# Kernel optimization log

Hardware: AMD Instinct MI355X
Metric: run time of the kernel (lower is better)

Reference implementation:

```python
import jax, jax.numpy as jnp
import numpy as np

B, H, W = 32, 512, 512
LAM = 1.0


def _pdist(x):
    # x: (n, d) -> (n, n) euclidean distance matrix (torch.cdist equivalent)
    sq = jnp.sum(x * x, axis=-1)
    d2 = sq[:, None] + sq[None, :] - 2.0 * (x @ x.T)
    return jnp.sqrt(jnp.maximum(d2, 0.0))


def _mst_edges(D):
    # 0-dim Vietoris-Rips persistence pairing == edges of the minimum spanning
    # tree of the distance matrix. Prim's algorithm, n-1 sequential steps.
    n = D.shape[0]
    big = jnp.asarray(jnp.finfo(D.dtype).max, D.dtype)
    in_tree = jnp.zeros(n, dtype=bool).at[0].set(True)
    min_dist = D[0].at[0].set(big)          # best distance from tree to each node
    min_from = jnp.zeros(n, dtype=jnp.int32)  # tree endpoint achieving min_dist

    def step(carry, _):
        in_tree, md, mf = carry
        j = jnp.argmin(jnp.where(in_tree, big, md)).astype(jnp.int32)
        i = mf[j]
        in_tree = in_tree.at[j].set(True)
        better = (D[j] < md) & (~in_tree)
        md = jnp.where(better, D[j], md)
        mf = jnp.where(better, j, mf)
        return (in_tree, md, mf), (i, j)

    _, (us, vs) = jax.lax.scan(step, (in_tree, min_dist, min_from), None, length=n - 1)
    return us, vs  # each (n-1,) int32


def _topo_loss_single(x, z):
    # x, z: (n, d) point clouds (prediction / mask rows as points)
    Dx = _pdist(x)
    Dz = _pdist(z)
    # SignatureLoss normalisation: divide distance matrices by their max
    Dx = Dx / jnp.maximum(Dx.max(), 1e-12)
    Dz = Dz / jnp.maximum(Dz.max(), 1e-12)
    # persistence pairings (dim 0) of each space
    ux, vx = _mst_edges(jax.lax.stop_gradient(Dx))
    uz, vz = _mst_edges(jax.lax.stop_gradient(Dz))
    # signature loss (Topological Autoencoders, p=2):
    # ||D_X[pi_X] - D_Z[pi_X]||_2^2 + ||D_X[pi_Z] - D_Z[pi_Z]||_2^2
    t1 = jnp.sum((Dx[ux, vx] - Dz[ux, vx]) ** 2)
    t2 = jnp.sum((Dx[uz, vz] - Dz[uz, vz]) ** 2)
    return t1 + t2


def setup_inputs() -> dict:
    key = jax.random.key(0)
    k1, k2 = jax.random.split(key)
    model_output = jax.random.normal(k1, (B, 1, H, W), dtype=jnp.float32)
    labels = jax.random.uniform(k2, (B, 1, H, W), dtype=jnp.float32)
    return {"model_output": model_output, "labels": labels}


def reference(model_output, labels):
    preds = jax.nn.sigmoid(jnp.squeeze(model_output, axis=1))  # (B, H, W)
    masks = jnp.squeeze(labels, axis=1)                        # (B, H, W)
    losses = jax.vmap(_topo_loss_single)(preds, masks)         # (B,)
    return LAM * jnp.sum(losses) / preds.shape[0]
```

## Files before the change

kernel.cpp:

```cpp
#include <hip/hip_runtime.h>
#include <math.h>

#define NN 512
#define NN2 (NN*NN)
#define NB 32
#define NM 64

typedef __attribute__((ext_vector_type(8))) short short8v;
typedef __attribute__((ext_vector_type(4))) float f32x4;

typedef const unsigned int __attribute__((address_space(1)))* gas_ptr;
typedef unsigned int __attribute__((address_space(3)))* las_ptr;

__device__ __forceinline__ float sigm(float x) { return 1.0f / (1.0f + expf(-x)); }

__device__ __forceinline__ unsigned short f2bf(float x) {
  unsigned u = __float_as_uint(x);
  return (unsigned short)((u + 0x7fffu + ((u >> 16) & 1u)) >> 16);
}
__device__ __forceinline__ float bf2f(unsigned short h) {
  return __uint_as_float(((unsigned)h) << 16);
}
__device__ __forceinline__ unsigned long long u64min(unsigned long long a,
                                                     unsigned long long b) {
  return (b < a) ? b : a;
}
__device__ __forceinline__ void amin64(unsigned long long* p, unsigned long long v) {
  unsigned long long old = *p;
  while (v < old) {
    unsigned long long assumed = old;
    old = atomicCAS(p, assumed, v);
    if (old == assumed) break;
  }
}
template <int CTRL>
__device__ __forceinline__ unsigned long long dpp_min_u64(unsigned long long x) {
  int xlo = (int)(unsigned)x, xhi = (int)(unsigned)(x >> 32);
  int ylo = __builtin_amdgcn_update_dpp(xlo, xlo, CTRL, 0xf, 0xf, false);
  int yhi = __builtin_amdgcn_update_dpp(xhi, xhi, CTRL, 0xf, 0xf, false);
  unsigned long long y = ((unsigned long long)(unsigned)yhi << 32) | (unsigned)ylo;
  return (y < x) ? y : x;
}
__device__ __forceinline__ unsigned long long wave_min_u64(unsigned long long k) {
  k = dpp_min_u64<0x111>(k); k = dpp_min_u64<0x112>(k);
  k = dpp_min_u64<0x114>(k); k = dpp_min_u64<0x118>(k);
  k = dpp_min_u64<0x142>(k); k = dpp_min_u64<0x143>(k);
  return k;
}
__device__ __forceinline__ unsigned long long grp16_min_u64(unsigned long long k) {
  k = dpp_min_u64<0x111>(k); k = dpp_min_u64<0x112>(k);
  k = dpp_min_u64<0x114>(k); k = dpp_min_u64<0x118>(k);
  return k;
}

__global__ __launch_bounds__(256) void split_kernel(const float* __restrict__ model,
                                                    const float* __restrict__ labels,
                                                    unsigned short* __restrict__ Hi,
                                                    unsigned short* __restrict__ Lo,
                                                    float* __restrict__ sq, int m0) {
  int b = blockIdx.x;
  int mL = b >> 8;
  int m = m0 + mL;
  int tid = threadIdx.x;
  size_t off = (size_t)(b & 255) * 1024 + tid * 4;
  const float* src = ((m & 1) ? labels + (size_t)(m >> 1) * NN2
                              : model + (size_t)(m >> 1) * NN2) + off;
  float4 v = *(const float4*)src;
  if (!(m & 1)) { v.x = sigm(v.x); v.y = sigm(v.y); v.z = sigm(v.z); v.w = sigm(v.w); }
  ushort4 h, l;
  h.x = f2bf(v.x); l.x = f2bf(v.x - bf2f(h.x));
  h.y = f2bf(v.y); l.y = f2bf(v.y - bf2f(h.y));
  h.z = f2bf(v.z); l.z = f2bf(v.z - bf2f(h.z));
  h.w = f2bf(v.w); l.w = f2bf(v.w - bf2f(h.w));
  *(ushort4*)(Hi + (size_t)mL * NN2 + off) = h;
  *(ushort4*)(Lo + (size_t)mL * NN2 + off) = l;
  float s = v.x * v.x + v.y * v.y + v.z * v.z + v.w * v.w;
  #pragma unroll
  for (int o = 32; o > 0; o >>= 1) s += __shfl_down(s, o);
  __shared__ float red[4];
  if ((tid & 63) == 0) red[tid >> 6] = s;
  __syncthreads();
  if (tid == 0) {
    int row0 = (b & 255) * 2;
    sq[(size_t)m * NN + row0]     = red[0] + red[1];
    sq[(size_t)m * NN + row0 + 1] = red[2] + red[3];
  }
}

__global__ __launch_bounds__(256, 3) void gemm_dist(const unsigned short* __restrict__ Hi,
                                                    const unsigned short* __restrict__ Lo,
                                                    const float* __restrict__ sq,
                                                    unsigned short* __restrict__ Dreg,
                                                    unsigned* __restrict__ maxBits,
                                                    unsigned long long* __restrict__ best1,
                                                    int m0, int nm) {
  __shared__ unsigned short P[4][4096];
  int id = blockIdx.x;
  int p, mL;
  if ((nm & 7) == 0) {
    int x = id & 7, t = id >> 3;
    p = t % 10;
    mL = x + 8 * (t / 10);
  } else {
    p = id % 10;
    mL = id / 10;
  }
  int by = (p >= 4) + (p >= 7) + (p >= 9);
  int bx = p - ((by * (7 - by)) >> 1);
  bool diag = (by == bx);
  int m = m0 + mL;
  const unsigned short* Hm = Hi + (size_t)mL * NN2;
  const unsigned short* Lm = Lo + (size_t)mL * NN2;

  int tid = threadIdx.x;
  int wid = tid >> 6, lane = tid & 63;
  int wy = wid >> 1, wx = wid & 1;
  int lr = lane & 15, lk = lane >> 4;

  const unsigned short* wsrcM = (wid & 1) ? Lm : Hm;
  int wrow0 = (wid < 2) ? by * 128 : bx * 128;
  bool stage = (!diag) || (wid < 2);
  int srow = lane >> 2;
  int schunk = (lane & 3) ^ ((lane >> 3) & 3);
  const unsigned short* gsrc = wsrcM + (size_t)(wrow0 + srow) * NN + schunk * 8;
  unsigned short* ldst = &P[wid & 3][0];

  f32x4 acc[4][4];
  #pragma unroll
  for (int i = 0; i < 4; ++i)
    #pragma unroll
    for (int j = 0; j < 4; ++j) acc[i][j] = (f32x4){0.f, 0.f, 0.f, 0.f};

  const unsigned short* bAh = &P[0][0];
  const unsigned short* bAl = &P[1][0];
  const unsigned short* bBh = diag ? &P[0][0] : &P[2][0];
  const unsigned short* bBl = diag ? &P[1][0] : &P[3][0];
  int sw = (lr >> 1) & 3;
  int rao = (wy * 64 + lr) * 32 + (lk ^ sw) * 8;
  int rbo = (wx * 64 + lr) * 32 + (lk ^ sw) * 8;

  for (int s = 0; s < 16; ++s) {
    int k0 = s * 32;
    if (stage) {
      #pragma unroll
      for (int i = 0; i < 8; ++i)
        __builtin_amdgcn_global_load_lds(
            (gas_ptr)(const void*)(gsrc + k0 + (size_t)i * 16 * NN),
            (las_ptr)(void*)(ldst + i * 512), 16, 0, 0);
    }
    __syncthreads();

    short8v fa[4], fb[4], fb2[4];
    #pragma unroll
    for (int i = 0; i < 4; ++i) {
      fa[i] = *(const short8v*)(bAh + rao + i * 512);
      fb[i] = *(const short8v*)(bBh + rbo + i * 512);
    }
    #pragma unroll
    for (int mi = 0; mi < 4; ++mi)
      #pragma unroll
      for (int ni = 0; ni < 4; ++ni)
        acc[mi][ni] = __builtin_amdgcn_mfma_f32_16x16x32_bf16(fa[mi], fb[ni], acc[mi][ni], 0, 0, 0);
    #pragma unroll
    for (int i = 0; i < 4; ++i)
      fb2[i] = *(const short8v*)(bBl + rbo + i * 512);
    #pragma unroll
    for (int mi = 0; mi < 4; ++mi)
      #pragma unroll
      for (int ni = 0; ni < 4; ++ni)
        acc[mi][ni] = __builtin_amdgcn_mfma_f32_16x16x32_bf16(fa[mi], fb2[ni], acc[mi][ni], 0, 0, 0);
    #pragma unroll
    for (int i = 0; i < 4; ++i)
      fa[i] = *(const short8v*)(bAl + rao + i * 512);
    #pragma unroll
    for (int mi = 0; mi < 4; ++mi)
      #pragma unroll
      for (int ni = 0; ni < 4; ++ni)
        acc[mi][ni] = __builtin_amdgcn_mfma_f32_16x16x32_bf16(fa[mi], fb[ni], acc[mi][ni], 0, 0, 0);
    __syncthreads();
  }

  const float* sqm = sq + (size_t)m * NN;
  unsigned short* Dm = Dreg + (size_t)mL * NN2;
  int gr0 = by * 128 + wy * 64;
  int gc0 = bx * 128 + wx * 64;
  unsigned hmax = 0;
  unsigned long long* b1 = best1 + (size_t)m * NN;
  unsigned long long ck[4];
  #pragma unroll
  for (int i = 0; i < 4; ++i) ck[i] = ~0ull;
  unsigned short us[4][4][4];

  #pragma unroll
  for (int mi = 0; mi < 4; ++mi) {
    int rb = gr0 + mi * 16 + lk * 4;
    float sqi0 = sqm[rb + 0], sqi1 = sqm[rb + 1], sqi2 = sqm[rb + 2], sqi3 = sqm[rb + 3];
    unsigned long long rk[4];
    #pragma unroll
    for (int j = 0; j < 4; ++j) rk[j] = ~0ull;
    #pragma unroll
    for (int ni = 0; ni < 4; ++ni) {
      int col = gc0 + ni * 16 + lr;
      float sqj = sqm[col];
      f32x4 a = acc[mi][ni];
      unsigned short h0 = f2bf(sqrtf(fmaxf(sqi0 + sqj - 2.f * a[0], 0.f)));
      unsigned short h1 = f2bf(sqrtf(fmaxf(sqi1 + sqj - 2.f * a[1], 0.f)));
      unsigned short h2 = f2bf(sqrtf(fmaxf(sqi2 + sqj - 2.f * a[2], 0.f)));
      unsigned short h3 = f2bf(sqrtf(fmaxf(sqi3 + sqj - 2.f * a[3], 0.f)));
      us[mi][ni][0] = h0; us[mi][ni][1] = h1;
      us[mi][ni][2] = h2; us[mi][ni][3] = h3;
      unsigned hm01 = (h0 > h1) ? h0 : h1;
      unsigned hm23 = (h2 > h3) ? h2 : h3;
      unsigned hm = (hm01 > hm23) ? hm01 : hm23;
      hmax = (hm > hmax) ? hm : hmax;
      unsigned short hh[4] = {h0, h1, h2, h3};
      #pragma unroll
      for (int rg = 0; rg < 4; ++rg) {
        int row = rb + rg;
        if (!diag || col != row) {
          unsigned lo = (row < col) ? (unsigned)(row * NN + col)
                                    : (unsigned)(col * NN + row);
          unsigned long long key = ((unsigned long long)hh[rg] << 48) | lo;
          rk[rg] = u64min(rk[rg], key);
          ck[ni] = u64min(ck[ni], key);
        }
      }
    }
    #pragma unroll
    for (int rg = 0; rg < 4; ++rg) {
      unsigned long long k = grp16_min_u64(rk[rg]);
      if (lr == 15) atomicMin(&b1[rb + rg], k);
    }
  }
  if (!diag) {
    #pragma unroll
    for (int ni = 0; ni < 4; ++ni) {
      unsigned long long k = ck[ni];
      k = u64min(k, __shfl_xor(k, 16));
      k = u64min(k, __shfl_xor(k, 32));
      if (lk == 0) atomicMin(&b1[gc0 + ni * 16 + lr], k);
    }
  }

  __syncthreads();
  unsigned short* W = &P[0][0] + wid * 1216;
  int rlo = lane >> 4, cq = lane & 15;
  #pragma unroll
  for (int mi = 0; mi < 4; ++mi) {
    #pragma unroll
    for (int ni = 0; ni < 4; ++ni)
      #pragma unroll
      for (int j = 0; j < 4; ++j)
        W[(lk * 4 + j) * 76 + ni * 16 + lr] = us[mi][ni][j];
    #pragma unroll
    for (int g = 0; g < 4; ++g) {
      int r16 = g * 4 + rlo;
      ushort4 t = *(const ushort4*)&W[r16 * 76 + cq * 4];
      *(ushort4*)(Dm + (size_t)(gr0 + mi * 16 + r16) * NN + gc0 + cq * 4) = t;
    }
  }
  if (!diag) {
    #pragma unroll
    for (int ni = 0; ni < 4; ++ni) {
      #pragma unroll
      for (int mi = 0; mi < 4; ++mi)
        *(ushort4*)&W[lr * 76 + mi * 16 + lk * 4] =
            make_ushort4(us[mi][ni][0], us[mi][ni][1], us[mi][ni][2], us[mi][ni][3]);
      #pragma unroll
      for (int g = 0; g < 4; ++g) {
        int r16 = g * 4 + rlo;
        ushort4 t = *(const ushort4*)&W[r16 * 76 + cq * 4];
        *(ushort4*)(Dm + (size_t)(gc0 + ni * 16 + r16) * NN + gr0 + cq * 4) = t;
      }
    }
  }

  #pragma unroll
  for (int off = 32; off > 0; off >>= 1) {
    unsigned o = (unsigned)__shfl_down((int)hmax, off);
    hmax = (o > hmax) ? o : hmax;
  }
  if (lane == 0) atomicMax(&maxBits[m], hmax << 16);
}

__global__ __launch_bounds__(512) void scan2_kernel(const unsigned short* __restrict__ Dreg,
                                                    const unsigned long long* __restrict__ best1,
                                                    int* __restrict__ compG,
                                                    unsigned long long* __restrict__ best2,
                                                    unsigned long long* __restrict__ DcG,
                                                    int2* __restrict__ eo_all,
                                                    int* __restrict__ ecntG, int m0) {
  int sblk = blockIdx.x, mL = blockIdx.y, m = m0 + mL;
  const unsigned short* D = Dreg + (size_t)mL * NN2;
  __shared__ int compP[NN + 64];
  __shared__ int hook[NN], parent[NN];
  __shared__ int ecnt;
  int tid = threadIdx.x;
  int wave = tid >> 6, lane = tid & 63;
  int c0 = lane * 8;

  unsigned long long* dginit = DcG + (size_t)mL * 16384 + sblk * 2048;
  #pragma unroll
  for (int i = 0; i < 4; ++i) dginit[tid + i * 512] = ~0ull;

  if (tid == 0) ecnt = 0;
  unsigned long long b = best1[(size_t)m * NN + tid];
  int h;
  if (b != ~0ull) {
    int idx = (int)(unsigned)b & 0x3ffff;
    int er = idx >> 9, ec = idx & 511;
    h = (er == tid) ? ec : er;
  } else h = tid;
  hook[tid] = h;
  __syncthreads();
  bool active = (b != ~0ull);
  int p = h;
  bool mutual = active && (hook[p] == tid);
  parent[tid] = (!active) ? tid : ((mutual && tid < p) ? tid : p);
  if (sblk == 0 && active && (!mutual || tid > p)) {
    int idx = (int)(unsigned)b & 0x3ffff;
    int e = atomicAdd(&ecnt, 1);
    eo_all[(size_t)m * (NN - 1) + e] = make_int2(idx >> 9, idx & 511);
  }
  __syncthreads();
  int c = tid, pp = parent[c];
  while (pp != c) { c = pp; pp = parent[c]; }
  compP[tid + (tid >> 3)] = c;
  if (sblk == 0) {
    compG[(size_t)m * NN + tid] = c;
    if (tid == 0) ecntG[m] = ecnt;
  }
  __syncthreads();

  unsigned long long* b2 = best2 + (size_t)m * NN;
  #pragma unroll
  for (int rr = 0; rr < 8; ++rr) {
    int r = sblk * 64 + wave * 8 + rr;
    int cr = compP[r + (r >> 3)];
    uint4 dv = *(const uint4*)(D + (size_t)r * NN + c0);
    int4 cc0 = *(const int4*)(compP + c0 + (c0 >> 3));
    int4 cc1 = *(const int4*)(compP + c0 + 4 + (c0 >> 3));
    unsigned hh[8] = {dv.x & 0xffffu, dv.x >> 16, dv.y & 0xffffu, dv.y >> 16,
                      dv.z & 0xffffu, dv.z >> 16, dv.w & 0xffffu, dv.w >> 16};
    int cv[8] = {cc0.x, cc0.y, cc0.z, cc0.w, cc1.x, cc1.y, cc1.z, cc1.w};
    unsigned long long k = ~0ull;
    #pragma unroll
    for (int e = 0; e < 8; ++e) {
      if (cv[e] != cr) {
        int col = c0 + e;
        int lo = (r < col) ? r * NN + col : col * NN + r;
        unsigned long long key = ((unsigned long long)hh[e] << 48) | (unsigned)lo;
        k = u64min(k, key);
      }
    }
    k = wave_min_u64(k);
    if (lane == 63 && k != ~0ull) atomicMin(&b2[cr], k);
  }
}

__global__ __launch_bounds__(512) void hook2_kernel(const unsigned long long* __restrict__ best2,
                                                    const int* __restrict__ compG,
                                                    int* __restrict__ comp2g,
                                                    int2* __restrict__ eo_all,
                                                    int* __restrict__ ecntG,
                                                    int* __restrict__ cntG, int m0) {
  int mL = blockIdx.x, m = m0 + mL;
  const unsigned long long* b2 = best2 + (size_t)m * NN;
  int2* eo = eo_all + (size_t)m * (NN - 1);
  __shared__ int comp[NN], hook[NN], parent[NN], dmap[NN];
  __shared__ int ecnt, ccnt;
  int tid = threadIdx.x;
  if (tid == 0) { ecnt = ecntG[m]; ccnt = 0; }
  comp[tid] = compG[(size_t)m * NN + tid];
  __syncthreads();
  unsigned long long b = b2[tid];
  int h;
  if (b != ~0ull) {
    int idx = (int)(unsigned)b & 0x3ffff;
    int er = idx >> 9, ec = idx & 511;
    int c1 = comp[er], c2 = comp[ec];
    h = (c1 == tid) ? c2 : c1;
  } else h = tid;
  hook[tid] = h;
  __syncthreads();
  bool active = (b != ~0ull);
  int p = h;
  bool mutual = active && (hook[p] == tid);
  parent[tid] = (!active) ? tid : ((mutual && tid < p) ? tid : p);
  if (active && (!mutual || tid > p)) {
    int idx = (int)(unsigned)b & 0x3ffff;
    int e = atomicAdd(&ecnt, 1);
    eo[e] = make_int2(idx >> 9, idx & 511);
  }
  __syncthreads();
  int c = comp[tid], pp = parent[c];
  while (pp != c) { c = pp; pp = parent[c]; }
  __syncthreads();
  comp[tid] = c;
  __syncthreads();
  if (comp[tid] == tid) dmap[tid] = atomicAdd(&ccnt, 1);
  __syncthreads();
  comp2g[(size_t)m * NN + tid] = dmap[comp[tid]];
  if (tid == 0) { ecntG[m] = ecnt; cntG[m] = ccnt; }
}

__global__ __launch_bounds__(512) void contract_kernel(const unsigned short* __restrict__ Dreg,
                                                       const int* __restrict__ comp2g,
                                                       unsigned long long* __restrict__ DcG,
                                                       int m0) {
  int q = blockIdx.x, mL = blockIdx.y, m = m0 + mL;
  const unsigned short* D = Dreg + (size_t)mL * NN2;
  __shared__ unsigned long long Dc[128 * 128];
  __shared__ int c2P[NN + 64];
  int tid = threadIdx.x;
  int wave = tid >> 6, lane = tid & 63;
  int c0 = lane * 8;
  if (tid < NN) c2P[tid + (tid >> 3)] = comp2g[(size_t)m * NN + tid];
  for (int i = tid; i < 16384; i += 512) Dc[i] = ~0ull;
  __syncthreads();
  #pragma unroll
  for (int rr = 0; rr < 16; ++rr) {
    int r = q * 128 + wave * 16 + rr;
    int di = c2P[r + (r >> 3)];
    uint4 dv = *(const uint4*)(D + (size_t)r * NN + c0);
    int4 cc0 = *(const int4*)(c2P + c0 + (c0 >> 3));
    int4 cc1 = *(const int4*)(c2P + c0 + 4 + (c0 >> 3));
    unsigned hh[8] = {dv.x & 0xffffu, dv.x >> 16, dv.y & 0xffffu, dv.y >> 16,
                      dv.z & 0xffffu, dv.z >> 16, dv.w & 0xffffu, dv.w >> 16};
    int cv[8] = {cc0.x, cc0.y, cc0.z, cc0.w, cc1.x, cc1.y, cc1.z, cc1.w};
    #pragma unroll
    for (int e = 0; e < 8; ++e) {
      if (cv[e] != di) {
        int col = c0 + e;
        int lo = (r < col) ? r * NN + col : col * NN + r;
        unsigned long long key = ((unsigned long long)hh[e] << 48) | (unsigned)lo;
        amin64(&Dc[di * 128 + cv[e]], key);
      }
    }
  }
  __syncthreads();
  unsigned long long* dg = DcG + (size_t)mL * 16384;
  for (int i = tid; i < 16384; i += 512) {
    unsigned long long v = Dc[i];
    if (v != ~0ull) atomicMin(&dg[i], v);
  }
}

__global__ __launch_bounds__(1024) void finish_kernel(const unsigned short* __restrict__ Dreg,
                                                      const unsigned long long* __restrict__ DcG,
                                                      const int* __restrict__ comp2g,
                                                      const int* __restrict__ cntG,
                                                      int2* __restrict__ eo_all,
                                                      int* __restrict__ ecntG,
                                                      const unsigned* __restrict__ maxBits,
                                                      float* __restrict__ out, int m0) {
  int mL = blockIdx.x, m = m0 + mL;
  __shared__ unsigned long long Dc[16384];
  __shared__ int c2n[NN];
  __shared__ unsigned long long best[128];
  __shared__ int comp2[128], hook128[128], parent128[128];
  __shared__ float fred[16];
  __shared__ int ecnt;
  int tid = threadIdx.x;
  int wave = tid >> 6, lane = tid & 63;
  const unsigned long long* dg = DcG + (size_t)mL * 16384;
  for (int i = tid; i < 16384; i += 1024) Dc[i] = dg[i];
  if (tid < NN) c2n[tid] = comp2g[(size_t)m * NN + tid];
  if (tid < 128) comp2[tid] = tid;
  if (tid == 0) ecnt = ecntG[m];
  __syncthreads();
  int C = cntG[m];
  int2* eo = eo_all + (size_t)m * (NN - 1);

  for (int ph = 0; ph < 7; ++ph) {
    if (ecnt >= NN - 1) break;
    if (tid < 128) best[tid] = ~0ull;
    __syncthreads();
    for (int i = tid; i < C * 128; i += 1024) {
      unsigned long long key = Dc[i];
      if (key == ~0ull) continue;
      int a = i >> 7, bb = i & 127;
      int ca = comp2[a], cb = comp2[bb];
      if (ca != cb) amin64(&best[ca], key);
    }
    __syncthreads();
    if (tid < C) {
      unsigned long long b = best[tid];
      int h;
      if (b != ~0ull) {
        int pid = (int)(unsigned)b & 0x3ffff;
        int er = pid >> 9, ec = pid & 511;
        int c1 = comp2[c2n[er]], c2v = comp2[c2n[ec]];
        h = (c1 == tid) ? c2v : c1;
      } else h = tid;
      hook128[tid] = h;
    }
    __syncthreads();
    if (tid < C) {
      unsigned long long b = best[tid];
      bool active = (b != ~0ull);
      int p = hook128[tid];
      bool mutual = active && (hook128[p] == tid);
      parent128[tid] = (!active) ? tid : ((mutual && tid < p) ? tid : p);
      if (active && (!mutual || tid > p)) {
        int pid = (int)(unsigned)b & 0x3ffff;
        int e = atomicAdd(&ecnt, 1);
        eo[e] = make_int2(pid >> 9, pid & 511);
      }
    }
    __syncthreads();
    if (tid < C) {
      int c = comp2[tid], pp = parent128[c];
      while (pp != c) { c = pp; pp = parent128[c]; }
      comp2[tid] = c;
    }
    __syncthreads();
  }
  __syncthreads();

  int b = m >> 1;
  float mxX = fmaxf(__uint_as_float(maxBits[2 * b]), 1e-12f);
  float mxZ = fmaxf(__uint_as_float(maxBits[2 * b + 1]), 1e-12f);
  float rX = 1.0f / mxX, rZ = 1.0f / mxZ;
  const unsigned short* Dx = Dreg + (size_t)(mL & ~1) * NN2;
  const unsigned short* Dz = Dx + NN2;
  float acc = 0.f;
  if (tid < NN - 1) {
    int2 e = eo[tid];
    size_t off = (size_t)e.x * NN + e.y;
    float d = bf2f(Dx[off]) * rX - bf2f(Dz[off]) * rZ;
    acc = d * d;
  }
  #pragma unroll
  for (int o = 32; o > 0; o >>= 1) acc += __shfl_down(acc, o);
  if (lane == 0) fred[wave] = acc;
  __syncthreads();
  if (tid == 0) {
    float t = 0.f;
    #pragma unroll
    for (int i = 0; i < 16; ++i) t += fred[i];
    atomicAdd(out, t * (1.0f / NB));
  }
}

extern "C" void kernel_launch(void* const* d_in, const int* in_sizes, int n_in,
                              void* d_out, int out_size, void* d_ws, size_t ws_size,
                              hipStream_t stream) {
  const float* model = (const float*)d_in[0];
  const float* labels = (const float*)d_in[1];
  float* out = (float*)d_out;
  char* ws = (char*)d_ws;

  float*              sq      = (float*)(ws);
  unsigned*           maxBits = (unsigned*)(ws + 131072);
  int2*               eo      = (int2*)(ws + 132096);
  unsigned long long* best1   = (unsigned long long*)(ws + 393728);
  unsigned long long* best2   = (unsigned long long*)(ws + 655872);
  int*                compG   = (int*)(ws + 918016);
  int*                comp2g  = (int*)(ws + 1049088);
  int*                ecntG   = (int*)(ws + 1180160);
  int*                cntG    = (int*)(ws + 1180416);
  size_t base = 1181696;

  size_t perBatch = 2ull * (NN2 * 2 + 2ull * NN2 * 2 + 16384 * 8);
  size_t dcap = (ws_size > base) ? (ws_size - base) : 0;
  int cb = (int)(dcap / perBatch);
  if (cb > NB) cb = NB;
  if (cb < 1) cb = 1;
  int nmc = 2 * cb;

  unsigned short* Dreg = (unsigned short*)(ws + base);
  unsigned short* Hi = Dreg + (size_t)nmc * NN2;
  unsigned short* Lo = Hi + (size_t)nmc * NN2;
  unsigned long long* DcG = (unsigned long long*)(Lo + (size_t)nmc * NN2);

  hipMemsetAsync(d_out, 0, sizeof(float), stream);
  hipMemsetAsync(maxBits, 0, 64 * sizeof(unsigned), stream);

  for (int b0 = 0; b0 < NB; b0 += cb) {
    int nb = (NB - b0 < cb) ? (NB - b0) : cb;
    int nm = 2 * nb, m0 = 2 * b0;
    hipMemsetAsync(best1 + (size_t)m0 * NN, 0xFF, (size_t)nm * NN * 16, stream);
    split_kernel<<<nm * 256, 256, 0, stream>>>(model, labels, Hi, Lo, sq, m0);
    gemm_dist<<<10 * nm, 256, 0, stream>>>(Hi, Lo, sq, Dreg, maxBits, best1, m0, nm);
    scan2_kernel<<<dim3(8, nm), 512, 0, stream>>>(Dreg, best1, compG, best2, DcG,
                                                  eo, ecntG, m0);
    hook2_kernel<<<nm, 512, 0, stream>>>(best2, compG, comp2g, eo, ecntG, cntG, m0);
    contract_kernel<<<dim3(4, nm), 512, 0, stream>>>(Dreg, comp2g, DcG, m0);
    finish_kernel<<<nm, 1024, 0, stream>>>(Dreg, DcG, comp2g, cntG, eo, ecntG,
                                           maxBits, out, m0);
  }
}
```

Baseline: 140.3 us.

## Fuse hook2 into contract and finish kernels, fold best-buffer reset into split

```diff
diff --git a/kernel.cpp b/kernel.cpp
--- a/kernel.cpp
+++ b/kernel.cpp
@@ -57,7 +57,10 @@
                                                     const float* __restrict__ labels,
                                                     unsigned short* __restrict__ Hi,
                                                     unsigned short* __restrict__ Lo,
-                                                    float* __restrict__ sq, int m0) {
+                                                    float* __restrict__ sq,
+                                                    unsigned long long* __restrict__ best1,
+                                                    unsigned long long* __restrict__ best2,
+                                                    int m0) {
   int b = blockIdx.x;
   int mL = b >> 8;
   int m = m0 + mL;
@@ -74,6 +77,13 @@
   h.w = f2bf(v.w); l.w = f2bf(v.w - bf2f(h.w));
   *(ushort4*)(Hi + (size_t)mL * NN2 + off) = h;
   *(ushort4*)(Lo + (size_t)mL * NN2 + off) = l;
+  if (tid == 0) {
+    int bi = (b & 255) * 2;
+    best1[(size_t)m * NN + bi]     = ~0ull;
+    best1[(size_t)m * NN + bi + 1] = ~0ull;
+    best2[(size_t)m * NN + bi]     = ~0ull;
+    best2[(size_t)m * NN + bi + 1] = ~0ull;
+  }
   float s = v.x * v.x + v.y * v.y + v.z * v.z + v.w * v.w;
   #pragma unroll
   for (int o = 32; o > 0; o >>= 1) s += __shfl_down(s, o);
@@ -358,66 +368,88 @@
   }
 }
 
-__global__ __launch_bounds__(512) void hook2_kernel(const unsigned long long* __restrict__ best2,
-                                                    const int* __restrict__ compG,
-                                                    int* __restrict__ comp2g,
-                                                    int2* __restrict__ eo_all,
-                                                    int* __restrict__ ecntG,
-                                                    int* __restrict__ cntG, int m0) {
-  int mL = blockIdx.x, m = m0 + mL;
-  const unsigned long long* b2 = best2 + (size_t)m * NN;
-  int2* eo = eo_all + (size_t)m * (NN - 1);
-  __shared__ int comp[NN], hook[NN], parent[NN], dmap[NN];
-  __shared__ int ecnt, ccnt;
-  int tid = threadIdx.x;
-  if (tid == 0) { ecnt = ecntG[m]; ccnt = 0; }
-  comp[tid] = compG[(size_t)m * NN + tid];
-  __syncthreads();
-  unsigned long long b = b2[tid];
-  int h;
-  if (b != ~0ull) {
+__device__ __forceinline__ void hook2_inline(const unsigned long long* b2m,
+                                             const int* compG_m, int tid, bool valid,
+                                             int wave, int lane, bool emit,
+                                             int2* eo, int* ecnt,
+                                             int* comp, int* hookA, int* parentA,
+                                             unsigned long long* rootMask,
+                                             int* denseOut, int* Cout) {
+  unsigned long long b = ~0ull;
+  if (valid) { comp[tid] = compG_m[tid]; b = b2m[tid]; }
+  __syncthreads();
+  int h = tid;
+  if (valid && b != ~0ull) {
     int idx = (int)(unsigned)b & 0x3ffff;
     int er = idx >> 9, ec = idx & 511;
     int c1 = comp[er], c2 = comp[ec];
     h = (c1 == tid) ? c2 : c1;
-  } else h = tid;
-  hook[tid] = h;
-  __syncthreads();
-  bool active = (b != ~0ull);
-  int p = h;
-  bool mutual = active && (hook[p] == tid);
-  parent[tid] = (!active) ? tid : ((mutual && tid < p) ? tid : p);
-  if (active && (!mutual || tid > p)) {
-    int idx = (int)(unsigned)b & 0x3ffff;
-    int e = atomicAdd(&ecnt, 1);
-    eo[e] = make_int2(idx >> 9, idx & 511);
-  }
-  __syncthreads();
-  int c = comp[tid], pp = parent[c];
-  while (pp != c) { c = pp; pp = parent[c]; }
-  __syncthreads();
-  comp[tid] = c;
-  __syncthreads();
-  if (comp[tid] == tid) dmap[tid] = atomicAdd(&ccnt, 1);
-  __syncthreads();
-  comp2g[(size_t)m * NN + tid] = dmap[comp[tid]];
-  if (tid == 0) { ecntG[m] = ecnt; cntG[m] = ccnt; }
+  }
+  if (valid) hookA[tid] = h;
+  __syncthreads();
+  if (valid) {
+    bool active = (b != ~0ull);
+    int p = h;
+    bool mutual = active && (hookA[p] == tid);
+    parentA[tid] = (!active) ? tid : ((mutual && tid < p) ? tid : p);
+    if (emit && active && (!mutual || tid > p)) {
+      int idx = (int)(unsigned)b & 0x3ffff;
+      int e = atomicAdd(ecnt, 1);
+      eo[e] = make_int2(idx >> 9, idx & 511);
+    }
+  }
+  __syncthreads();
+  int c = 0;
+  bool isRoot = false;
+  if (valid) {
+    c = comp[tid];
+    int pp = parentA[c];
+    while (pp != c) { c = pp; pp = parentA[c]; }
+    isRoot = (c == tid);
+  }
+  unsigned long long rm = __ballot(isRoot);
+  if (valid && lane == 0) rootMask[wave] = rm;
+  __syncthreads();
+  int cw = c >> 6, cl = c & 63;
+  int dense = 0, C = 0;
+  #pragma unroll
+  for (int w = 0; w < 8; ++w) {
+    int pc = __popcll(rootMask[w]);
+    C += pc;
+    if (w < cw) dense += pc;
+  }
+  dense += __popcll(rootMask[cw] & (cl ? ((~0ull) >> (64 - cl)) : 0ull));
+  *denseOut = dense;
+  *Cout = C;
 }
 
 __global__ __launch_bounds__(512) void contract_kernel(const unsigned short* __restrict__ Dreg,
-                                                       const int* __restrict__ comp2g,
+                                                       const unsigned long long* __restrict__ best2,
+                                                       const int* __restrict__ compG,
                                                        unsigned long long* __restrict__ DcG,
-                                                       int m0) {
+                                                       int2* __restrict__ eo_all,
+                                                       int* __restrict__ ecntG, int m0) {
   int q = blockIdx.x, mL = blockIdx.y, m = m0 + mL;
   const unsigned short* D = Dreg + (size_t)mL * NN2;
   __shared__ unsigned long long Dc[128 * 128];
+  __shared__ int comp[NN], hookA[NN], parentA[NN];
   __shared__ int c2P[NN + 64];
+  __shared__ unsigned long long rootMask[8];
+  __shared__ int ecnt;
   int tid = threadIdx.x;
   int wave = tid >> 6, lane = tid & 63;
   int c0 = lane * 8;
-  if (tid < NN) c2P[tid + (tid >> 3)] = comp2g[(size_t)m * NN + tid];
   for (int i = tid; i < 16384; i += 512) Dc[i] = ~0ull;
-  __syncthreads();
+  if (tid == 0) ecnt = ecntG[m];
+  __syncthreads();
+  int dense, C;
+  hook2_inline(best2 + (size_t)m * NN, compG + (size_t)m * NN, tid, true, wave, lane,
+               q == 0, eo_all + (size_t)m * (NN - 1), &ecnt,
+               comp, hookA, parentA, rootMask, &dense, &C);
+  c2P[tid + (tid >> 3)] = dense;
+  __syncthreads();
+  if (q == 0 && tid == 0) ecntG[m] = ecnt;
+
   #pragma unroll
   for (int rr = 0; rr < 16; ++rr) {
     int r = q * 128 + wave * 16 + rr;
@@ -448,8 +480,8 @@
 
 __global__ __launch_bounds__(1024) void finish_kernel(const unsigned short* __restrict__ Dreg,
                                                       const unsigned long long* __restrict__ DcG,
-                                                      const int* __restrict__ comp2g,
-                                                      const int* __restrict__ cntG,
+                                                      const unsigned long long* __restrict__ best2,
+                                                      const int* __restrict__ compG,
                                                       int2* __restrict__ eo_all,
                                                       int* __restrict__ ecntG,
                                                       const unsigned* __restrict__ maxBits,
@@ -457,19 +489,29 @@
   int mL = blockIdx.x, m = m0 + mL;
   __shared__ unsigned long long Dc[16384];
   __shared__ int c2n[NN];
+  __shared__ int comp[NN], hookA[NN], parentA[NN];
+  __shared__ unsigned long long rootMask[8];
   __shared__ unsigned long long best[128];
   __shared__ int comp2[128], hook128[128], parent128[128];
   __shared__ float fred[16];
-  __shared__ int ecnt;
+  __shared__ int ecnt, Csh;
   int tid = threadIdx.x;
   int wave = tid >> 6, lane = tid & 63;
   const unsigned long long* dg = DcG + (size_t)mL * 16384;
   for (int i = tid; i < 16384; i += 1024) Dc[i] = dg[i];
-  if (tid < NN) c2n[tid] = comp2g[(size_t)m * NN + tid];
   if (tid < 128) comp2[tid] = tid;
   if (tid == 0) ecnt = ecntG[m];
   __syncthreads();
-  int C = cntG[m];
+  {
+    int dense, C;
+    hook2_inline(best2 + (size_t)m * NN, compG + (size_t)m * NN, tid, tid < NN,
+                 wave, lane, false, nullptr, nullptr,
+                 comp, hookA, parentA, rootMask, &dense, &C);
+    if (tid < NN) c2n[tid] = dense;
+    if (tid == 0) Csh = C;
+  }
+  __syncthreads();
+  int C = Csh;
   int2* eo = eo_all + (size_t)m * (NN - 1);
 
   for (int ph = 0; ph < 7; ++ph) {
@@ -557,10 +599,8 @@
   unsigned long long* best1   = (unsigned long long*)(ws + 393728);
   unsigned long long* best2   = (unsigned long long*)(ws + 655872);
   int*                compG   = (int*)(ws + 918016);
-  int*                comp2g  = (int*)(ws + 1049088);
-  int*                ecntG   = (int*)(ws + 1180160);
-  int*                cntG    = (int*)(ws + 1180416);
-  size_t base = 1181696;
+  int*                ecntG   = (int*)(ws + 1049088);
+  size_t base = 1050624;
 
   size_t perBatch = 2ull * (NN2 * 2 + 2ull * NN2 * 2 + 16384 * 8);
   size_t dcap = (ws_size > base) ? (ws_size - base) : 0;
@@ -580,14 +620,14 @@
   for (int b0 = 0; b0 < NB; b0 += cb) {
     int nb = (NB - b0 < cb) ? (NB - b0) : cb;
     int nm = 2 * nb, m0 = 2 * b0;
-    hipMemsetAsync(best1 + (size_t)m0 * NN, 0xFF, (size_t)nm * NN * 16, stream);
-    split_kernel<<<nm * 256, 256, 0, stream>>>(model, labels, Hi, Lo, sq, m0);
+    split_kernel<<<nm * 256, 256, 0, stream>>>(model, labels, Hi, Lo, sq,
+                                               best1, best2, m0);
     gemm_dist<<<10 * nm, 256, 0, stream>>>(Hi, Lo, sq, Dreg, maxBits, best1, m0, nm);
     scan2_kernel<<<dim3(8, nm), 512, 0, stream>>>(Dreg, best1, compG, best2, DcG,
                                                   eo, ecntG, m0);
-    hook2_kernel<<<nm, 512, 0, stream>>>(best2, compG, comp2g, eo, ecntG, cntG, m0);
-    contract_kernel<<<dim3(4, nm), 512, 0, stream>>>(Dreg, comp2g, DcG, m0);
-    finish_kernel<<<nm, 1024, 0, stream>>>(Dreg, DcG, comp2g, cntG, eo, ecntG,
+    contract_kernel<<<dim3(4, nm), 512, 0, stream>>>(Dreg, best2, compG, DcG,
+                                                     eo, ecntG, m0);
+    finish_kernel<<<nm, 1024, 0, stream>>>(Dreg, DcG, best2, compG, eo, ecntG,
                                            maxBits, out, m0);
   }
 }
```

Measured after the change: 136.9 us. 2.4% less time.
